# Performance work log

Hardware: AMD Instinct MI355X
Metric: run time of the kernel (lower is better)

Reference implementation:

```python
import jax, jax.numpy as jnp
import numpy as np

DN = ('NCHW', 'OIHW', 'NCHW')

def conv(x, w, b=None):
    y = jax.lax.conv_general_dilated(x, w, (1, 1), 'SAME', dimension_numbers=DN)
    if b is not None:
        y = y + b[None, :, None, None]
    return y

def bn(x, g, b, m, v, eps=1e-5):
    inv = jax.lax.rsqrt(v + eps)
    return (x - m[None, :, None, None]) * (g * inv)[None, :, None, None] + b[None, :, None, None]

def _wind_kernels():
    iso = np.array([[0.1, 0.2, 0.1], [0.2, 1.0, 0.2], [0.1, 0.2, 0.1]], np.float32)
    diag = np.array([[0.1, 0.1, 0.1], [0.1, 1.0, 0.3], [0.1, 0.1, 0.1]], np.float32)
    # directions: N, NE, E, SE, S, SW, W, NW
    ks = [iso if d in (0, 2, 4, 6) else diag for d in range(8)]
    return jnp.asarray(np.stack(ks)[:, None])  # [8,1,3,3]

def setup_inputs() -> dict:
    key = jax.random.key(0)
    ks = jax.random.split(key, 32)
    B, C, H, W = 16, 22, 256, 256
    hid = 64
    env = jax.random.normal(ks[0], (B, C, H, W), jnp.float32)
    # make wind channels realistic so the gated wind path activates
    env = env.at[:, 7].set(jax.random.uniform(ks[1], (B, H, W)) * 360.0)   # direction deg
    env = env.at[:, 8].set(jax.random.uniform(ks[2], (B, H, W)) * 20.0)    # speed
    fire0 = jax.random.uniform(ks[3], (B, 1, H, W), jnp.float32)

    def w(k, shape):
        return jax.random.normal(k, shape, jnp.float32) * 0.05

    def bnp(k, c):
        k1, k2, k3, k4 = jax.random.split(k, 4)
        return (1.0 + 0.1 * jax.random.normal(k1, (c,)),
                0.1 * jax.random.normal(k2, (c,)),
                0.1 * jax.random.normal(k3, (c,)),
                0.5 + jax.random.uniform(k4, (c,)))

    g1, be1, m1, v1 = bnp(ks[6], hid)
    g2, be2, m2, v2 = bnp(ks[7], hid)
    cg1, cbe1, cm1, cv1 = bnp(ks[8], hid)
    cg2, cbe2, cm2, cv2 = bnp(ks[9], hid // 2)
    return dict(
        env_features=env, initial_fire_state=fire0,
        w1=w(ks[10], (hid, C, 3, 3)), b1=w(ks[11], (hid,)),
        g1=g1, be1=be1, m1=m1, v1=v1,
        w2=w(ks[12], (hid, hid, 3, 3)), b2=w(ks[13], (hid,)),
        g2=g2, be2=be2, m2=m2, v2=v2,
        cw1=w(ks[14], (hid, hid + 4, 3, 3)), cb1=w(ks[15], (hid,)),
        cg1=cg1, cbe1=cbe1, cm1=cm1, cv1=cv1,
        cw2=w(ks[16], (hid // 2, hid, 3, 3)), cb2=w(ks[17], (hid // 2,)),
        cg2=cg2, cbe2=cbe2, cm2=cm2, cv2=cv2,
        cw3=w(ks[18], (4, hid // 2, 1, 1)), cb3=w(ks[19], (4,)),
        wind_k=_wind_kernels(),
        num_steps=5,
    )

def reference(env_features, initial_fire_state,
              w1, b1, g1, be1, m1, v1,
              w2, b2, g2, be2, m2, v2,
              cw1, cb1, cg1, cbe1, cm1, cv1,
              cw2, cb2, cg2, cbe2, cm2, cv2,
              cw3, cb3, wind_k, num_steps):
    # env encoder
    env = jax.nn.relu(bn(conv(env_features, w1, b1), g1, be1, m1, v1))
    env = jax.nn.relu(bn(conv(env, w2, b2), g2, be2, m2, v2))

    # per-batch wind gating: fully vectorized over batch x 8 directions
    wind_angle = env_features[:, 7].mean(axis=(1, 2))            # [B]
    wind_speed = env_features[:, 8].mean(axis=(1, 2))            # [B]
    dir_angles = jnp.arange(8, dtype=jnp.float32) * 45.0         # [8]
    diff = jnp.abs(wind_angle[:, None] - dir_angles[None, :])
    diff = jnp.minimum(diff, 360.0 - diff)
    dw = jnp.maximum(0.0, 1.0 - diff / 90.0)                     # [B,8]
    ws = jnp.clip(wind_speed / 20.0, 0.0, 1.0)                   # [B]
    gate = (dw > 0.1) & (ws[:, None] > 0.1)
    eff = jnp.where(gate, dw * ws[:, None], 0.0)                 # [B,8]

    fire_state = initial_fire_state
    evolution = [fire_state]
    for _ in range(num_steps):
        # encode fire state as one-hot of {unburned, burning, burned, water}
        idx = jnp.where(fire_state < 0.25, 0, jnp.where(fire_state < 0.75, 1, 2))
        one_hot = jax.nn.one_hot(idx[:, 0], 4, dtype=fire_state.dtype)  # [B,H,W,4]
        one_hot = jnp.transpose(one_hot, (0, 3, 1, 2))                  # [B,4,H,W]

        ca_in = jnp.concatenate([env, one_hot], axis=1)
        h = jax.nn.relu(bn(conv(ca_in, cw1, cb1), cg1, cbe1, cm1, cv1))
        h = jax.nn.relu(bn(conv(h, cw2, cb2), cg2, cbe2, cm2, cv2))
        logits = conv(h, cw3, cb3)                                      # [B,4,H,W]
        probs = jax.nn.softmax(logits, axis=1)

        # wind influence: one batched depthwise-style conv over 8 directions
        we = conv(fire_state, wind_k)                                   # [B,8,H,W]
        wind_inf = jnp.einsum('bd,bdhw->bhw', eff, we)[:, None]         # [B,1,H,W]

        boost = jax.nn.sigmoid(wind_inf) * 0.3
        target = (probs[:, 1:2] + boost) * 0.5 + probs[:, 2:3] * 1.0
        fire_state = jnp.clip(0.7 * fire_state + 0.3 * target, 0.0, 1.0)
        evolution.append(fire_state)

    return fire_state, jnp.stack(evolution, axis=0)
```

## Files before the change

kernel.cpp:

```cpp
#include <hip/hip_runtime.h>
#include <cstdint>
#include <cstddef>


#define HWSZ 65536

typedef _Float16 f16;
typedef f16 f16x8 __attribute__((ext_vector_type(8)));
typedef f16 f16x4 __attribute__((ext_vector_type(4)));
typedef float f32x4 __attribute__((ext_vector_type(4)));

#define GLDS16(gp, lp)                                                        \
  __builtin_amdgcn_global_load_lds(                                           \
      (const __attribute__((address_space(1))) void*)(gp),                    \
      (__attribute__((address_space(3))) void*)(lp), 16, 0, 0)

__global__ void k_wprepC0(const float* __restrict__ src, f16* __restrict__ dst) {
  int i = blockIdx.x * 256 + threadIdx.x;
  if (i >= 64 * 288) return;
  int co = i / 288, k = i - co * 288;
  int tap = k >> 5, ci = k & 31;
  float v = 0.f;
  if (ci < 22) {
    v = src[(co * 22 + ci) * 9 + tap];
    if (ci == 7) v *= 64.f;
  }
  dst[i] = (f16)v;
}

__global__ void k_wprep64(const float* __restrict__ src, f16* __restrict__ dst,
                          int COUT) {
  int i = blockIdx.x * 256 + threadIdx.x;
  if (i >= COUT * 576) return;
  int co = i / 576, k = i - co * 576;
  int tap = k >> 6, ci = k & 63;
  dst[i] = (f16)src[(co * 64 + ci) * 9 + tap];
}

__global__ void k_wprepC1env(const float* __restrict__ src, f16* __restrict__ dst) {
  int i = blockIdx.x * 256 + threadIdx.x;
  if (i >= 64 * 576) return;
  int co = i / 576, k = i - co * 576;
  int tap = k >> 6, ci = k & 63;
  dst[i] = (f16)src[(co * 68 + ci) * 9 + tap];
}

__global__ void k_wprepOh(const float* __restrict__ src, f16* __restrict__ dst) {
  int i = blockIdx.x * 256 + threadIdx.x;
  if (i >= 9 * 5 * 72) return;
  int tap = i / (5 * 72), r = i - tap * (5 * 72);
  int cls = r / 72, co = r - cls * 72;
  float v = 0.f;
  if (co < 64 && cls < 4) v = src[(co * 68 + 64 + cls) * 9 + tap];
  dst[i] = (f16)v;
}

__global__ void k_wprepC1(const float* __restrict__ src, f16* __restrict__ dst) {
  int i = blockIdx.x * 256 + threadIdx.x;
  if (i >= 64 * 640) return;
  int co = i / 640, k = i - co * 640;
  float v;
  if (k < 576) {
    int tap = k >> 6, ci = k & 63;
    v = src[(co * 68 + ci) * 9 + tap];
  } else {
    int kl = k - 576;
    int oc = kl & 3, tp = kl >> 2;
    v = (tp < 9) ? src[(co * 68 + 64 + oc) * 9 + tp] : 0.f;
  }
  dst[i] = (f16)v;
}

__global__ void k_bnfuse(const float* __restrict__ g, const float* __restrict__ be,
                         const float* __restrict__ m, const float* __restrict__ v,
                         const float* __restrict__ bc, float* __restrict__ s,
                         float* __restrict__ t, int C) {
  int c = threadIdx.x;
  if (c < C) {
    float sc = g[c] * rsqrtf(v[c] + 1e-5f);
    s[c] = sc;
    t[c] = (bc[c] - m[c]) * sc + be[c];
  }
}

__global__ void k_ident(float* __restrict__ s, float* __restrict__ t) {
  int c = threadIdx.x;
  if (c < 64) { s[c] = 1.f; t[c] = 0.f; }
}

__global__ __launch_bounds__(256) void k_windpart(const float* __restrict__ env,
                                                  double* __restrict__ part) {
  int blk = blockIdx.x;
  int b = blk >> 5, j = blk & 31;
  const float4* a7 = (const float4*)(env + (((size_t)(b * 22 + 7)) << 16) + j * 2048);
  const float4* a8 = (const float4*)(env + (((size_t)(b * 22 + 8)) << 16) + j * 2048);
  int tid = threadIdx.x;
  double s7 = 0.0, s8 = 0.0;
  for (int i = tid; i < 512; i += 256) {
    float4 v = a7[i];
    s7 += (double)v.x + (double)v.y + (double)v.z + (double)v.w;
    float4 u = a8[i];
    s8 += (double)u.x + (double)u.y + (double)u.z + (double)u.w;
  }
  __shared__ double r7[256], r8[256];
  r7[tid] = s7; r8[tid] = s8;
  __syncthreads();
  for (int off = 128; off > 0; off >>= 1) {
    if (tid < off) { r7[tid] += r7[tid + off]; r8[tid] += r8[tid + off]; }
    __syncthreads();
  }
  if (tid == 0) {
    part[(b * 32 + j) * 2 + 0] = r7[0];
    part[(b * 32 + j) * 2 + 1] = r8[0];
  }
}

__global__ void k_windfin(const double* __restrict__ part,
                          const float* __restrict__ wind_k, float* __restrict__ wke) {
  int b = blockIdx.x;
  if (threadIdx.x != 0) return;
  double s7 = 0.0, s8 = 0.0;
  for (int j = 0; j < 32; ++j) {
    s7 += part[(b * 32 + j) * 2 + 0];
    s8 += part[(b * 32 + j) * 2 + 1];
  }
  float wa = (float)(s7 * (1.0 / 65536.0));
  float wsp = (float)(s8 * (1.0 / 65536.0));
  float wsc = fminf(fmaxf(wsp * (1.f / 20.f), 0.f), 1.f);
  float wk[9];
#pragma unroll
  for (int tp = 0; tp < 9; ++tp) wk[tp] = 0.f;
  for (int d = 0; d < 8; ++d) {
    float diff = fabsf(wa - 45.f * (float)d);
    diff = fminf(diff, 360.f - diff);
    float dw = fmaxf(0.f, 1.f - diff * (1.f / 90.f));
    float eff = (dw > 0.1f && wsc > 0.1f) ? dw * wsc : 0.f;
    for (int tp = 0; tp < 9; ++tp) wk[tp] += eff * wind_k[d * 9 + tp];
  }
  for (int tp = 0; tp < 9; ++tp) wke[b * 9 + tp] = wk[tp];
}

__global__ void k_copy(const float* __restrict__ src, float* __restrict__ dst) {
  int i = blockIdx.x * 256 + threadIdx.x;
  ((float4*)dst)[i] = ((const float4*)src)[i];
}

__global__ void k_border(f16* __restrict__ buf, int nimg, int C) {
  int i = blockIdx.x * 256 + threadIdx.x;
  int per = 1028 * C;
  if (i >= nimg * per) return;
  int img = i / per, r = i - img * per;
  int px = r / C, c = r - px * C;
  int h, w;
  if (px < 258) { h = 0; w = px; }
  else if (px < 516) { h = 257; w = px - 258; }
  else if (px < 772) { h = px - 515; w = 0; }
  else { h = px - 771; w = 257; }
  buf[((size_t)(img * 258 + h) * 258 + w) * C + c] = (f16)0.f;
}

__global__ __launch_bounds__(256) void k_env2h(const float* __restrict__ env,
                                               f16* __restrict__ dst, int nimg) {
  int i = blockIdx.x * 256 + threadIdx.x;
  if (i >= (nimg << 16)) return;
  int b = i >> 16, hw = i & 65535;
  int h = hw >> 8, w = hw & 255;
  const float* sp = env + (((size_t)b * 22) << 16) + hw;
  f16 o[32];
#pragma unroll
  for (int c = 0; c < 22; ++c) {
    float v = sp[(size_t)c << 16];
    if (c == 7) v *= (1.f / 64.f);
    o[c] = (f16)v;
  }
#pragma unroll
  for (int c = 22; c < 32; ++c) o[c] = (f16)0.f;
  f16* dp = dst + ((size_t)(b * 258 + h + 1) * 258 + (w + 1)) * 32;
  *(f16x8*)(dp + 0) = *(f16x8*)&o[0];
  *(f16x8*)(dp + 8) = *(f16x8*)&o[8];
  *(f16x8*)(dp + 16) = *(f16x8*)&o[16];
  *(f16x8*)(dp + 24) = *(f16x8*)&o[24];
}

__global__ void k_firemap(const float* __restrict__ fire, unsigned char* __restrict__ map,
                          int nimg) {
  int i = blockIdx.x * 256 + threadIdx.x;
  if (i >= nimg * 66564) return;
  int b = i / 66564, r = i - b * 66564;
  int h = r / 258, w = r - h * 258;
  unsigned char v = 4;
  if (h >= 1 && h <= 256 && w >= 1 && w <= 256) {
    float f = fire[((size_t)b << 16) + ((h - 1) << 8) + (w - 1)];
    v = f < 0.25f ? 0 : (f < 0.75f ? 1 : 2);
  }
  map[i] = v;
}

template <int CIN, int NCS, int NS, bool ONEHOT, bool OUTPAD, bool PXSPLIT, bool RELU>
__global__ __launch_bounds__(128, 2) void k_convM(
    const f16* __restrict__ x, const f16* __restrict__ Wp,
    const float* __restrict__ scale, const float* __restrict__ shift,
    const unsigned char* __restrict__ fmap, f16* __restrict__ y, int NB) {
  constexpr int COUT = PXSPLIT ? NCS * 16 : NCS * 32;
  constexpr int KT = NS * 32;
  constexpr int CC = CIN / 8;
  constexpr int PERROW = 34 * CC;
  constexpr int ROWE = 34 * CIN;
  constexpr int PXW = PXSPLIT ? 1 : 2;
  constexpr int NH = CIN / 32;
  constexpr int VN0 = (CIN == 64) ? 6 : 4;
  constexpr int VN1 = (CIN == 64) ? 4 : 2;

  __shared__ __align__(16) f16 xs[8][ROWE];
  __shared__ float sst[2][COUT];

  int tid = threadIdx.x;
  int lane = tid & 63;
  int l15 = lane & 15;
  int g = (lane >> 4) & 3;
  int wco = tid >> 6;

  int d = blockIdx.x;
  int hsn = NB * 8;
  int ws = d / hsn;
  int t = d - ws * hsn;
  int b = t >> 3;
  int hs = t & 7;
  int w0 = ws * 32, h0 = hs * 32;

  int co_base = PXSPLIT ? 0 : wco * NCS * 16;
  int pxg = PXSPLIT ? wco * 16 : 0;

  f16x8 Af[NCS][NS];
  {
    const f16* wb = Wp + (size_t)(co_base + l15) * KT + g * 8;
#pragma unroll
    for (int cs = 0; cs < NCS; ++cs)
#pragma unroll
      for (int s = 0; s < NS; ++s)
        Af[cs][s] = *(const f16x8*)(wb + cs * 16 * KT + s * 32);
  }
  if (tid < COUT) {
    sst[0][tid] = scale[tid];
    sst[1][tid] = shift[tid];
  }

  auto stage_row = [&](int row) {
    int rs = row > 256 ? 256 : row;
    const f16* src = x + ((size_t)(b * 258 + rs + 1) * 258 + w0) * CIN;
    f16* dst = xs[(row + 1) & 7];
    for (int c = tid; c < PERROW; c += 128) {
      int px = c / CC, cc = c - px * CC;
      int sz = (CIN == 64) ? (px & 7) : ((px >> 1) & 3);
      GLDS16(src + px * CIN + ((cc ^ sz) << 3), dst + c * 8);
    }
  };

#define PHASE_SYNC()                                                      \
  do {                                                                    \
    if (wco == 0)                                                         \
      asm volatile("s_waitcnt vmcnt(%0)" ::"i"(VN0) : "memory");          \
    else                                                                  \
      asm volatile("s_waitcnt vmcnt(%0)" ::"i"(VN1) : "memory");          \
    __builtin_amdgcn_s_barrier();                                         \
    __builtin_amdgcn_sched_barrier(0);                                    \
  } while (0)

  stage_row(h0 - 1); stage_row(h0);
  stage_row(h0 + 1); stage_row(h0 + 2);
  stage_row(h0 + 3); stage_row(h0 + 4);
  PHASE_SYNC();

#pragma unroll 1
  for (int hp = h0; hp < h0 + 32; hp += 2) {
#pragma unroll
    for (int r2 = 0; r2 < 2; ++r2) {
      stage_row(hp + 5 + r2);
      int h = hp + r2;

      f32x4 acc[NCS][PXW];
#pragma unroll
      for (int cs = 0; cs < NCS; ++cs)
#pragma unroll
        for (int p = 0; p < PXW; ++p) acc[cs][p] = (f32x4){0.f, 0.f, 0.f, 0.f};

      int ia[PXW], ib[PXW], ic[PXW];
      if (ONEHOT) {
        int ta = 2 * g, tb = ta + 1;
        int dya = ta / 3, dxa = ta - 3 * dya;
        int dyb = tb / 3, dxb = tb - 3 * dyb;
#pragma unroll
        for (int pxb = 0; pxb < PXW; ++pxb) {
          int pxa = pxg + pxb * 16 + l15;
          ia[pxb] = fmap[(size_t)(b * 258 + h + dya) * 258 + w0 + pxa + dxa];
          ib[pxb] = fmap[(size_t)(b * 258 + h + dyb) * 258 + w0 + pxa + dxb];
          ic[pxb] = fmap[(size_t)(b * 258 + h + 2) * 258 + w0 + pxa + 2];
        }
      }

      const f16* sp0 = xs[h & 7];
      const f16* sp1 = xs[(h + 1) & 7];
      const f16* sp2 = xs[(h + 2) & 7];
#pragma unroll
      for (int tap = 0; tap < 9; ++tap) {
        const int dy = tap / 3, dx = tap - 3 * (tap / 3);
        const f16* sp = (dy == 0) ? sp0 : ((dy == 1) ? sp1 : sp2);
#pragma unroll
        for (int pxb = 0; pxb < PXW; ++pxb) {
          int pxd = pxg + pxb * 16 + l15 + dx;
          int sz = (CIN == 64) ? (pxd & 7) : ((pxd >> 1) & 3);
#pragma unroll
          for (int half = 0; half < NH; ++half) {
            f16x8 bb = *(const f16x8*)(sp + pxd * CIN + (((g + 4 * half) ^ sz) << 3));
#pragma unroll
            for (int cs = 0; cs < NCS; ++cs)
              acc[cs][pxb] = __builtin_amdgcn_mfma_f32_16x16x32_f16(
                  Af[cs][tap * NH + half], bb, acc[cs][pxb], 0, 0, 0);
          }
        }
      }
      if (ONEHOT) {
#pragma unroll
        for (int pxb = 0; pxb < PXW; ++pxb) {
          f16x8 b18, b19;
#pragma unroll
          for (int j = 0; j < 4; ++j) {
            b18[j] = (f16)((ia[pxb] == j) ? 1.f : 0.f);
            b18[j + 4] = (f16)((ib[pxb] == j) ? 1.f : 0.f);
            b19[j] = (f16)((g == 0 && ic[pxb] == j) ? 1.f : 0.f);
            b19[j + 4] = (f16)0.f;
          }
#pragma unroll
          for (int cs = 0; cs < NCS; ++cs) {
            acc[cs][pxb] = __builtin_amdgcn_mfma_f32_16x16x32_f16(
                Af[cs][NS - 2], b18, acc[cs][pxb], 0, 0, 0);
            acc[cs][pxb] = __builtin_amdgcn_mfma_f32_16x16x32_f16(
                Af[cs][NS - 1], b19, acc[cs][pxb], 0, 0, 0);
          }
        }
      }
#pragma unroll
      for (int cs = 0; cs < NCS; ++cs) {
        int cb = co_base + cs * 16 + 4 * g;
        f32x4 sv = *(const f32x4*)&sst[0][cb];
        f32x4 tv = *(const f32x4*)&sst[1][cb];
#pragma unroll
        for (int pxb = 0; pxb < PXW; ++pxb) {
          int px = pxg + pxb * 16 + l15;
          f16x4 o;
#pragma unroll
          for (int r = 0; r < 4; ++r) {
            float v = acc[cs][pxb][r] * sv[r] + tv[r];
            o[r] = (f16)(RELU ? fmaxf(v, 0.f) : v);
          }
          size_t oi =
              OUTPAD ? ((size_t)(b * 258 + h + 1) * 258 + (w0 + px + 1)) * 64 + cb
                     : ((size_t)(b * 256 + h) * 256 + (w0 + px)) * COUT + cb;
          *(f16x4*)&y[oi] = o;
        }
      }
    }
    PHASE_SYNC();
  }
#undef PHASE_SYNC
}

__global__ __launch_bounds__(128, 2) void k_convF(
    const f16* __restrict__ base, const f16* __restrict__ Wp,
    const f16* __restrict__ Woh,
    const float* __restrict__ s1v, const float* __restrict__ t1v,
    const float* __restrict__ s2v, const float* __restrict__ t2v,
    const unsigned char* __restrict__ fmap, f16* __restrict__ y, int NB) {
  constexpr int NS = 18, KT = NS * 32;
  __shared__ __align__(16) f16 xs[6][34 * 64];
  __shared__ f16 tbl[9 * 5 * 72];
  __shared__ float sA[2][64];
  __shared__ float sB[2][32];

  int tid = threadIdx.x;
  int lane = tid & 63;
  int l15 = lane & 15;
  int g = (lane >> 4) & 3;
  int wco = tid >> 6;

  int d = blockIdx.x;
  int hsn = NB * 8;
  int ws = d / hsn;
  int t = d - ws * hsn;
  int b = t >> 3;
  int hs = t & 7;
  int w0 = ws * 32, h0 = hs * 32;
  int co_base = wco * 16;

  f16x8 Af[NS];
  {
    const f16* wb = Wp + (size_t)(co_base + l15) * KT + g * 8;
#pragma unroll
    for (int s = 0; s < NS; ++s) Af[s] = *(const f16x8*)(wb + s * 32);
  }
  for (int i = tid; i < 9 * 5 * 72; i += 128) tbl[i] = Woh[i];
  if (tid < 64) sA[0][tid] = s1v[tid];
  else sA[1][tid - 64] = t1v[tid - 64];
  if (tid < 32) sB[0][tid] = s2v[tid];
  else if (tid < 64) sB[1][tid - 32] = t2v[tid - 32];
  __syncthreads();

  const unsigned char* fmb = fmap + (size_t)b * 66564;

  auto stage_pair = [&](int rbase) {
    for (int c = tid; c < 544; c += 128) {
      int r2 = c >= 272 ? 1 : 0;
      int cc = c - r2 * 272;
      int px = cc >> 3, q = cc & 7;
      int row = rbase + r2;
      int col = w0 - 1 + px;
      f16* dst = &xs[(row + 1) % 6][px * 64 + ((q ^ (px & 7)) << 3)];
      if ((unsigned)row < 256u && (unsigned)col < 256u) {
        f16x8 a = *(const f16x8*)&base[(((size_t)(b * 256 + row)) * 256 + col) * 64 + q * 8];
        int cls[9];
#pragma unroll
        for (int tap = 0; tap < 9; ++tap)
          cls[tap] = fmb[(size_t)(row + tap / 3) * 258 + col + tap % 3];
#pragma unroll
        for (int tap = 0; tap < 9; ++tap)
          a = a + *(const f16x8*)&tbl[(tap * 5 + cls[tap]) * 72 + q * 8];
        f16x8 o;
#pragma unroll
        for (int j = 0; j < 8; ++j) {
          float v = (float)a[j] * sA[0][q * 8 + j] + sA[1][q * 8 + j];
          o[j] = (f16)fmaxf(v, 0.f);
        }
        *(f16x8*)dst = o;
      } else {
        f16x8 z = {};
        *(f16x8*)dst = z;
      }
    }
  };

  stage_pair(h0 - 1);
  stage_pair(h0 + 1);
  __syncthreads();

#pragma unroll 1
  for (int hp = h0; hp < h0 + 32; hp += 2) {
    int c0 = 4 * tid;
    int rM2 = c0 >= 272 ? 1 : 0;
    int ccM = c0 - rM2 * 272;
    int pxM = ccM >> 3, qM = ccM & 7;
    int rowM = hp + 3 + rM2;
    int colM = w0 - 1 + pxM;
    bool okM = ((unsigned)rowM < 256u) && ((unsigned)colM < 256u);
    f16x8 sm0 = {}, sm1 = {}, sm2 = {}, sm3 = {};
    if (okM) {
      const f16* bp = &base[(((size_t)(b * 256 + rowM)) * 256 + colM) * 64 + qM * 8];
      sm0 = *(const f16x8*)(bp + 0);
      sm1 = *(const f16x8*)(bp + 8);
      sm2 = *(const f16x8*)(bp + 16);
      sm3 = *(const f16x8*)(bp + 24);
    }
    int px4 = 0, q4 = 0, col4 = 0;
    bool ok4 = false;
    f16x8 se = {};
    if (tid < 32) {
      int cc4 = 240 + tid;
      px4 = cc4 >> 3; q4 = cc4 & 7;
      col4 = w0 - 1 + px4;
      ok4 = ((unsigned)(hp + 4) < 256u) && ((unsigned)col4 < 256u);
      if (ok4)
        se = *(const f16x8*)&base[(((size_t)(b * 256 + hp + 4)) * 256 + col4) * 64 + q4 * 8];
    }
    __builtin_amdgcn_sched_barrier(0);

#pragma unroll
    for (int rr = 0; rr < 2; ++rr) {
      int h = hp + rr;
      f32x4 acc[2];
      acc[0] = (f32x4){0.f, 0.f, 0.f, 0.f};
      acc[1] = (f32x4){0.f, 0.f, 0.f, 0.f};
      const f16* sp0 = xs[h % 6];
      const f16* sp1 = xs[(h + 1) % 6];
      const f16* sp2 = xs[(h + 2) % 6];
#pragma unroll
      for (int tap = 0; tap < 9; ++tap) {
        const int dy = tap / 3, dx = tap - 3 * (tap / 3);
        const f16* sp = (dy == 0) ? sp0 : ((dy == 1) ? sp1 : sp2);
#pragma unroll
        for (int pxb = 0; pxb < 2; ++pxb) {
          int pxd = pxb * 16 + l15 + dx;
          int sz = pxd & 7;
#pragma unroll
          for (int half = 0; half < 2; ++half) {
            f16x8 bb = *(const f16x8*)(sp + pxd * 64 + (((g + 4 * half) ^ sz) << 3));
            acc[pxb] = __builtin_amdgcn_mfma_f32_16x16x32_f16(
                Af[tap * 2 + half], bb, acc[pxb], 0, 0, 0);
          }
        }
      }
      int cb = co_base + 4 * g;
      f32x4 sv = *(const f32x4*)&sB[0][cb];
      f32x4 tv = *(const f32x4*)&sB[1][cb];
#pragma unroll
      for (int pxb = 0; pxb < 2; ++pxb) {
        int px = pxb * 16 + l15;
        f16x4 o;
#pragma unroll
        for (int r = 0; r < 4; ++r)
          o[r] = (f16)fmaxf(acc[pxb][r] * sv[r] + tv[r], 0.f);
        *(f16x4*)&y[((size_t)(b * 256 + h) * 256 + (w0 + px)) * 32 + cb] = o;
      }
    }
    __builtin_amdgcn_sched_barrier(0);

    {
      f16* dstM = &xs[(rowM + 1) % 6][pxM * 64];
      if (okM) {
        int cls[9];
#pragma unroll
        for (int tap = 0; tap < 9; ++tap)
          cls[tap] = fmb[(size_t)(rowM + tap / 3) * 258 + colM + tap % 3];
#define XFORM(SRC, QOFF)                                                      \
  {                                                                           \
    int q_ = qM + QOFF;                                                       \
    f16x8 a_ = SRC;                                                           \
    _Pragma("unroll") for (int tap = 0; tap < 9; ++tap)                       \
        a_ = a_ + *(const f16x8*)&tbl[(tap * 5 + cls[tap]) * 72 + q_ * 8];    \
    f16x8 o_;                                                                 \
    _Pragma("unroll") for (int j = 0; j < 8; ++j) {                           \
      float v_ = (float)a_[j] * sA[0][q_ * 8 + j] + sA[1][q_ * 8 + j];        \
      o_[j] = (f16)fmaxf(v_, 0.f);                                           \
    }                                                                         \
    *(f16x8*)(dstM + ((q_ ^ (pxM & 7)) << 3)) = o_;                           \
  }
        XFORM(sm0, 0)
        XFORM(sm1, 1)
        XFORM(sm2, 2)
        XFORM(sm3, 3)
#undef XFORM
      } else {
        f16x8 z = {};
        *(f16x8*)(dstM + (((qM + 0) ^ (pxM & 7)) << 3)) = z;
        *(f16x8*)(dstM + (((qM + 1) ^ (pxM & 7)) << 3)) = z;
        *(f16x8*)(dstM + (((qM + 2) ^ (pxM & 7)) << 3)) = z;
        *(f16x8*)(dstM + (((qM + 3) ^ (pxM & 7)) << 3)) = z;
      }
      if (tid < 32) {
        f16* dst4 = &xs[(hp + 5) % 6][px4 * 64 + ((q4 ^ (px4 & 7)) << 3)];
        if (ok4) {
          int cls[9];
#pragma unroll
          for (int tap = 0; tap < 9; ++tap)
            cls[tap] = fmb[(size_t)(hp + 4 + tap / 3) * 258 + col4 + tap % 3];
          f16x8 a_ = se;
#pragma unroll
          for (int tap = 0; tap < 9; ++tap)
            a_ = a_ + *(const f16x8*)&tbl[(tap * 5 + cls[tap]) * 72 + q4 * 8];
          f16x8 o_;
#pragma unroll
          for (int j = 0; j < 8; ++j) {
            float v_ = (float)a_[j] * sA[0][q4 * 8 + j] + sA[1][q4 * 8 + j];
            o_[j] = (f16)fmaxf(v_, 0.f);
          }
          *(f16x8*)dst4 = o_;
        } else {
          f16x8 z = {};
          *(f16x8*)dst4 = z;
        }
      }
    }
    __syncthreads();
  }
}

__global__ __launch_bounds__(256) void k_step(
    const f16* __restrict__ h2, const float* __restrict__ cw3,
    const float* __restrict__ cb3, const float* __restrict__ wke,
    const float* __restrict__ fin, float* __restrict__ fout,
    float* __restrict__ fout2, unsigned char* __restrict__ mapout) {
  __shared__ float wl[4][32];
  __shared__ float bl[4];
  __shared__ float wk[9];
  int tid = threadIdx.x;
  if (tid < 128) wl[tid >> 5][tid & 31] = cw3[tid];
  if (tid < 4) bl[tid] = cb3[tid];
  int bx = blockIdx.x;
  int b = bx >> 8, h = bx & 255;
  if (tid < 9) wk[tid] = wke[b * 9 + tid];
  __syncthreads();
  int w = tid;
  const f16x8* hp8 = (const f16x8*)(h2 + ((size_t)(b * 256 + h) * 256 + w) * 32);
  float l0 = bl[0], l1 = bl[1], l2 = bl[2], l3 = bl[3];
#pragma unroll
  for (int q = 0; q < 4; ++q) {
    f16x8 v8 = hp8[q];
#pragma unroll
    for (int j = 0; j < 8; ++j) {
      float v = (float)v8[j];
      int c = q * 8 + j;
      l0 += v * wl[0][c];
      l1 += v * wl[1][c];
      l2 += v * wl[2][c];
      l3 += v * wl[3][c];
    }
  }
  float mx = fmaxf(fmaxf(l0, l1), fmaxf(l2, l3));
  float e0 = expf(l0 - mx), e1 = expf(l1 - mx), e2 = expf(l2 - mx), e3 = expf(l3 - mx);
  float inv = 1.f / (e0 + e1 + e2 + e3);
  float p1 = e1 * inv, p2 = e2 * inv;
  const float* fp = fin + ((size_t)b << 16);
  float wacc = 0.f;
#pragma unroll
  for (int tap = 0; tap < 9; ++tap) {
    int dy = tap / 3 - 1, dx = tap % 3 - 1;
    int hh = h + dy, ww2 = w + dx;
    float f = ((unsigned)hh < 256u && (unsigned)ww2 < 256u) ? fp[(hh << 8) + ww2] : 0.f;
    wacc += wk[tap] * f;
  }
  float boost = 0.3f / (1.f + expf(-wacc));
  float fcur = fp[(h << 8) + w];
  float target = 0.5f * p1 + 0.5f * boost + p2;
  float fn = 0.7f * fcur + 0.3f * target;
  fn = fminf(fmaxf(fn, 0.f), 1.f);
  size_t o = ((size_t)b << 16) + (h << 8) + w;
  fout[o] = fn;
  if (fout2) fout2[o] = fn;
  mapout[(size_t)(b * 258 + h + 1) * 258 + (w + 1)] =
      fn < 0.25f ? (unsigned char)0 : (fn < 0.75f ? (unsigned char)1 : (unsigned char)2);
}

extern "C" void kernel_launch(void* const* d_in, const int* in_sizes, int n_in,
                              void* d_out, int out_size, void* d_ws, size_t ws_size,
                              hipStream_t stream) {
  const float* env = (const float*)d_in[0];
  const float* fire0 = (const float*)d_in[1];
  const float* w1 = (const float*)d_in[2];
  const float* b1 = (const float*)d_in[3];
  const float* g1 = (const float*)d_in[4];
  const float* be1 = (const float*)d_in[5];
  const float* m1 = (const float*)d_in[6];
  const float* v1 = (const float*)d_in[7];
  const float* w2 = (const float*)d_in[8];
  const float* b2 = (const float*)d_in[9];
  const float* g2 = (const float*)d_in[10];
  const float* be2 = (const float*)d_in[11];
  const float* m2 = (const float*)d_in[12];
  const float* v2 = (const float*)d_in[13];
  const float* cw1 = (const float*)d_in[14];
  const float* cb1 = (const float*)d_in[15];
  const float* cg1 = (const float*)d_in[16];
  const float* cbe1 = (const float*)d_in[17];
  const float* cm1 = (const float*)d_in[18];
  const float* cv1 = (const float*)d_in[19];
  const float* cw2 = (const float*)d_in[20];
  const float* cb2 = (const float*)d_in[21];
  const float* cg2 = (const float*)d_in[22];
  const float* cbe2 = (const float*)d_in[23];
  const float* cm2 = (const float*)d_in[24];
  const float* cv2 = (const float*)d_in[25];
  const float* cw3 = (const float*)d_in[26];
  const float* cb3 = (const float*)d_in[27];
  const float* windk = (const float*)d_in[28];

  float* out = (float*)d_out;
  float* evo = out + 1048576;

  uint8_t* p = (uint8_t*)d_ws;
  f16* W1p = (f16*)p;           p += 64 * 288 * 2;
  f16* W2p = (f16*)p;           p += 64 * 576 * 2;
  f16* Wc1p = (f16*)p;          p += 64 * 640 * 2;
  f16* Wenv = (f16*)p;          p += 64 * 576 * 2;
  f16* Woh = (f16*)p;           p += 9 * 5 * 72 * 2;
  f16* Wc2p = (f16*)p;          p += 32 * 576 * 2;
  float* s1 = (float*)p;        p += 64 * 4;
  float* t1 = (float*)p;        p += 64 * 4;
  float* s2 = (float*)p;        p += 64 * 4;
  float* t2 = (float*)p;        p += 64 * 4;
  float* sc1 = (float*)p;       p += 64 * 4;
  float* tc1 = (float*)p;       p += 64 * 4;
  float* sc2 = (float*)p;       p += 64 * 4;
  float* tc2 = (float*)p;       p += 64 * 4;
  float* idsc = (float*)p;      p += 64 * 4;
  float* idsh = (float*)p;      p += 64 * 4;
  float* wke = (float*)p;       p += 1024;
  double* wpart = (double*)p;   p += 16 * 32 * 2 * 8;
  unsigned char* fmap = p;      p += 16 * 66564 + 1024;

  const size_t IMGP = (size_t)258 * 258 * 64;
  const size_t IMGP32 = (size_t)258 * 258 * 32;
  const size_t IMGU = (size_t)65536 * 64;
  const size_t S = 16 * IMGP * 2;
  const size_t CH64 = IMGP * 2;
  const size_t CH32 = IMGP32 * 2;
  size_t fixed = (size_t)(p - (uint8_t*)d_ws);

  bool basePath = false;
  int NB = 1;
  for (int nb = 16; nb >= 1; nb >>= 1) {
    if (fixed + 2 * S + (size_t)nb * CH32 <= ws_size) { basePath = true; NB = nb; break; }
  }
  if (!basePath) {
    for (int nb = 16; nb >= 1; nb >>= 1) {
      size_t need = fixed + S + (size_t)nb * (CH64 + CH32);
      if (need <= ws_size) { NB = nb; break; }
    }
  }

  k_wprepC0<<<(64 * 288 + 255) / 256, 256, 0, stream>>>(w1, W1p);
  k_wprep64<<<(64 * 576 + 255) / 256, 256, 0, stream>>>(w2, W2p, 64);
  k_wprep64<<<(32 * 576 + 255) / 256, 256, 0, stream>>>(cw2, Wc2p, 32);
  k_bnfuse<<<1, 256, 0, stream>>>(g1, be1, m1, v1, b1, s1, t1, 64);
  k_bnfuse<<<1, 256, 0, stream>>>(g2, be2, m2, v2, b2, s2, t2, 64);
  k_bnfuse<<<1, 256, 0, stream>>>(cg1, cbe1, cm1, cv1, cb1, sc1, tc1, 64);
  k_bnfuse<<<1, 256, 0, stream>>>(cg2, cbe2, cm2, cv2, cb2, sc2, tc2, 32);
  k_windpart<<<512, 256, 0, stream>>>(env, wpart);
  k_windfin<<<16, 64, 0, stream>>>(wpart, windk, wke);
  k_copy<<<1024, 256, 0, stream>>>(fire0, evo);
  k_firemap<<<(16 * 66564 + 255) / 256, 256, 0, stream>>>(fire0, fmap, 16);

  if (basePath) {
    k_wprepC1env<<<(64 * 576 + 255) / 256, 256, 0, stream>>>(cw1, Wenv);
    k_wprepOh<<<(9 * 5 * 72 + 255) / 256, 256, 0, stream>>>(cw1, Woh);
    k_ident<<<1, 64, 0, stream>>>(idsc, idsh);

    f16* S1 = (f16*)(p);
    f16* S2 = (f16*)(p + S);
    f16* chunk = (f16*)(p + 2 * S);
    f16* envin = chunk;
    f16* h2 = chunk;

    k_border<<<(16 * 1028 * 64 + 255) / 256, 256, 0, stream>>>(S1, 16, 64);
    k_border<<<(16 * 1028 * 64 + 255) / 256, 256, 0, stream>>>(S2, 16, 64);
    k_border<<<(NB * 1028 * 32 + 255) / 256, 256, 0, stream>>>(envin, NB, 32);

    const int gconv = NB * 64;
    for (int b0 = 0; b0 < 16; b0 += NB) {
      k_env2h<<<NB * 256, 256, 0, stream>>>(env + (size_t)b0 * 22 * HWSZ, envin, NB);
      k_convM<32, 2, 9, false, true, false, true><<<gconv, 128, 0, stream>>>(
          envin, W1p, s1, t1, nullptr, S1 + (size_t)b0 * IMGP, NB);
      k_convM<64, 2, 18, false, true, false, true><<<gconv, 128, 0, stream>>>(
          S1 + (size_t)b0 * IMGP, W2p, s2, t2, nullptr, S2 + (size_t)b0 * IMGP, NB);
      k_convM<64, 2, 18, false, false, false, false><<<gconv, 128, 0, stream>>>(
          S2 + (size_t)b0 * IMGP, Wenv, idsc, idsh, nullptr,
          S1 + (size_t)b0 * IMGU, NB);
    }
    for (int t = 0; t < 5; ++t) {
      const float* fin = evo + (size_t)t * 1048576;
      float* fo = evo + (size_t)(t + 1) * 1048576;
      for (int b0 = 0; b0 < 16; b0 += NB) {
        k_convF<<<gconv, 128, 0, stream>>>(
            S1 + (size_t)b0 * IMGU, Wc2p, Woh, sc1, tc1, sc2, tc2,
            fmap + (size_t)b0 * 66564, h2, NB);
        k_step<<<NB * 256, 256, 0, stream>>>(
            h2, cw3, cb3, wke + (size_t)b0 * 9, fin + (size_t)b0 * HWSZ,
            fo + (size_t)b0 * HWSZ, (t == 4) ? out + (size_t)b0 * HWSZ : nullptr,
            fmap + (size_t)b0 * 66564);
      }
    }
  } else {
    k_wprepC1<<<(64 * 640 + 255) / 256, 256, 0, stream>>>(cw1, Wc1p);
    f16* envf = (f16*)p;
    f16* h1p = (f16*)(p + S);
    f16* chunk = (f16*)(p + S + (size_t)NB * CH64);
    f16* envin = chunk;
    f16* h2 = chunk;

    k_border<<<(16 * 1028 * 64 + 255) / 256, 256, 0, stream>>>(envf, 16, 64);
    k_border<<<(NB * 1028 * 64 + 255) / 256, 256, 0, stream>>>(h1p, NB, 64);
    k_border<<<(NB * 1028 * 32 + 255) / 256, 256, 0, stream>>>(envin, NB, 32);

    const int gconv = NB * 64;
    for (int b0 = 0; b0 < 16; b0 += NB) {
      k_env2h<<<NB * 256, 256, 0, stream>>>(env + (size_t)b0 * 22 * HWSZ, envin, NB);
      k_convM<32, 2, 9, false, true, false, true><<<gconv, 128, 0, stream>>>(
          envin, W1p, s1, t1, nullptr, h1p, NB);
      k_convM<64, 2, 18, false, true, false, true><<<gconv, 128, 0, stream>>>(
          h1p, W2p, s2, t2, nullptr, envf + (size_t)b0 * IMGP, NB);
    }
    for (int t = 0; t < 5; ++t) {
      const float* fin = evo + (size_t)t * 1048576;
      float* fo = evo + (size_t)(t + 1) * 1048576;
      for (int b0 = 0; b0 < 16; b0 += NB) {
        k_convM<64, 2, 20, true, true, false, true><<<gconv, 128, 0, stream>>>(
            envf + (size_t)b0 * IMGP, Wc1p, sc1, tc1, fmap + (size_t)b0 * 66564,
            h1p, NB);
        k_convM<64, 2, 18, false, false, true, true><<<gconv, 128, 0, stream>>>(
            h1p, Wc2p, sc2, tc2, nullptr, h2, NB);
        k_step<<<NB * 256, 256, 0, stream>>>(
            h2, cw3, cb3, wke + (size_t)b0 * 9, fin + (size_t)b0 * HWSZ,
            fo + (size_t)b0 * HWSZ, (t == 4) ? out + (size_t)b0 * HWSZ : nullptr,
            fmap + (size_t)b0 * 66564);
      }
    }
  }
}
```

Baseline: 855.0 us.

## Split conv work across four waves per block with one output tile per wave

Adds a 256-thread k_convM4 variant in which each of four waves computes 16 output channels over the full 32-pixel row tile. It stages eight rows ahead through async global-to-LDS loads with per-wave vmcnt waits. k_convF also moves to 256 threads, splitting work as 2 channel groups times 2 pixel halves so each wave holds one accumulator, and its halo staging is simplified into shared load and transform helpers. The goal is more waves per CU to hide latency and less register pressure per wave. The cost is more threads contending for LDS and barriers, plus weight fragments reloaded per wave.

Result: slower. 1.779 ms (+108.0%).

```diff
diff --git a/kernel.cpp b/kernel.cpp
--- a/kernel.cpp
+++ b/kernel.cpp
@@ -194,6 +194,128 @@
     v = f < 0.25f ? 0 : (f < 0.75f ? 1 : 2);
   }
   map[i] = v;
+}
+
+template <int CIN, int NS, bool OUTPAD, bool RELU>
+__global__ __launch_bounds__(256, 4) void k_convM4(
+    const f16* __restrict__ x, const f16* __restrict__ Wp,
+    const float* __restrict__ scale, const float* __restrict__ shift,
+    f16* __restrict__ y, int NB) {
+  constexpr int KT = NS * 32;
+  constexpr int CC = CIN / 8;
+  constexpr int PERROW = 34 * CC;
+  constexpr int ROWE = 34 * CIN;
+  constexpr int NH = CIN / 32;
+  constexpr int NST = 4;
+  constexpr int SGA = (CIN == 64) ? 4 : 2;
+  constexpr int SGB = (CIN == 64) ? 2 : 0;
+
+  __shared__ __align__(16) f16 xs[8][ROWE];
+  __shared__ float sst[2][64];
+
+  int tid = threadIdx.x;
+  int lane = tid & 63;
+  int l15 = lane & 15;
+  int g = (lane >> 4) & 3;
+  int wid = tid >> 6;
+  bool lead = (CIN == 64) ? (wid == 0) : (wid < 3);
+  int co_base = wid * 16;
+
+  int d = blockIdx.x;
+  int hsn = NB * 8;
+  int ws = d / hsn;
+  int t = d - ws * hsn;
+  int b = t >> 3;
+  int hs = t & 7;
+  int w0 = ws * 32, h0 = hs * 32;
+
+  f16x8 Af[NS];
+  {
+    const f16* wb = Wp + (size_t)(co_base + l15) * KT + g * 8;
+#pragma unroll
+    for (int s = 0; s < NS; ++s) Af[s] = *(const f16x8*)(wb + s * 32);
+  }
+  if (tid < 64) sst[0][tid] = scale[tid];
+  else if (tid < 128) sst[1][tid - 64] = shift[tid - 64];
+
+  auto stage_row = [&](int row) {
+    int rs = row > 256 ? 256 : row;
+    const f16* src = x + ((size_t)(b * 258 + rs + 1) * 258 + w0) * CIN;
+    f16* dst = xs[(row + 1) & 7];
+    for (int c = tid; c < PERROW; c += 256) {
+      int px = c / CC, cc = c - px * CC;
+      int sz = (CIN == 64) ? (px & 7) : ((px >> 1) & 3);
+      GLDS16(src + px * CIN + ((cc ^ sz) << 3), dst + c * 8);
+    }
+  };
+
+#define PHASE_SYNC(NA, NBW)                                               \
+  do {                                                                    \
+    if (lead)                                                             \
+      asm volatile("s_waitcnt vmcnt(%0)" ::"i"(NA) : "memory");           \
+    else                                                                  \
+      asm volatile("s_waitcnt vmcnt(%0)" ::"i"(NBW) : "memory");          \
+    __builtin_amdgcn_s_barrier();                                         \
+    __builtin_amdgcn_sched_barrier(0);                                    \
+  } while (0)
+
+  stage_row(h0 - 1); stage_row(h0);
+  stage_row(h0 + 1); stage_row(h0 + 2);
+  stage_row(h0 + 3); stage_row(h0 + 4);
+  PHASE_SYNC(SGA, SGB);
+
+#pragma unroll 1
+  for (int hp = h0; hp < h0 + 32; hp += 2) {
+    stage_row(hp + 5);
+    stage_row(hp + 6);
+    __builtin_amdgcn_sched_barrier(0);
+
+#pragma unroll
+    for (int rr = 0; rr < 2; ++rr) {
+      int h = hp + rr;
+      f32x4 acc[2];
+      acc[0] = (f32x4){0.f, 0.f, 0.f, 0.f};
+      acc[1] = (f32x4){0.f, 0.f, 0.f, 0.f};
+      const f16* sp0 = xs[h & 7];
+      const f16* sp1 = xs[(h + 1) & 7];
+      const f16* sp2 = xs[(h + 2) & 7];
+#pragma unroll
+      for (int tap = 0; tap < 9; ++tap) {
+        const int dy = tap / 3, dx = tap - 3 * (tap / 3);
+        const f16* sp = (dy == 0) ? sp0 : ((dy == 1) ? sp1 : sp2);
+#pragma unroll
+        for (int pxb = 0; pxb < 2; ++pxb) {
+          int pxd = pxb * 16 + l15 + dx;
+          int sz = (CIN == 64) ? (pxd & 7) : ((pxd >> 1) & 3);
+#pragma unroll
+          for (int half = 0; half < NH; ++half) {
+            f16x8 bb = *(const f16x8*)(sp + pxd * CIN + (((g + 4 * half) ^ sz) << 3));
+            acc[pxb] = __builtin_amdgcn_mfma_f32_16x16x32_f16(
+                Af[tap * NH + half], bb, acc[pxb], 0, 0, 0);
+          }
+        }
+      }
+      int cb = co_base + 4 * g;
+      f32x4 sv = *(const f32x4*)&sst[0][cb];
+      f32x4 tv = *(const f32x4*)&sst[1][cb];
+#pragma unroll
+      for (int pxb = 0; pxb < 2; ++pxb) {
+        int px = pxb * 16 + l15;
+        f16x4 o;
+#pragma unroll
+        for (int r = 0; r < 4; ++r) {
+          float v = acc[pxb][r] * sv[r] + tv[r];
+          o[r] = (f16)(RELU ? fmaxf(v, 0.f) : v);
+        }
+        size_t oi =
+            OUTPAD ? ((size_t)(b * 258 + h + 1) * 258 + (w0 + px + 1)) * 64 + cb
+                   : ((size_t)(b * 256 + h) * 256 + (w0 + px)) * 64 + cb;
+        *(f16x4*)&y[oi] = o;
+      }
+    }
+    PHASE_SYNC(SGA + NST, SGB + NST);
+  }
+#undef PHASE_SYNC
 }
 
 template <int CIN, int NCS, int NS, bool ONEHOT, bool OUTPAD, bool PXSPLIT, bool RELU>
@@ -365,7 +487,7 @@
 #undef PHASE_SYNC
 }
 
-__global__ __launch_bounds__(128, 2) void k_convF(
+__global__ __launch_bounds__(256, 4) void k_convF(
     const f16* __restrict__ base, const f16* __restrict__ Wp,
     const f16* __restrict__ Woh,
     const float* __restrict__ s1v, const float* __restrict__ t1v,
@@ -381,7 +503,9 @@
   int lane = tid & 63;
   int l15 = lane & 15;
   int g = (lane >> 4) & 3;
-  int wco = tid >> 6;
+  int wid = tid >> 6;
+  int co_base = (wid & 1) * 16;
+  int pxg = (wid >> 1) * 16;
 
   int d = blockIdx.x;
   int hsn = NB * 8;
@@ -390,7 +514,6 @@
   int b = t >> 3;
   int hs = t & 7;
   int w0 = ws * 32, h0 = hs * 32;
-  int co_base = wco * 16;
 
   f16x8 Af[NS];
   {
@@ -398,86 +521,68 @@
 #pragma unroll
     for (int s = 0; s < NS; ++s) Af[s] = *(const f16x8*)(wb + s * 32);
   }
-  for (int i = tid; i < 9 * 5 * 72; i += 128) tbl[i] = Woh[i];
+  for (int i = tid; i < 9 * 5 * 72; i += 256) tbl[i] = Woh[i];
   if (tid < 64) sA[0][tid] = s1v[tid];
-  else sA[1][tid - 64] = t1v[tid - 64];
-  if (tid < 32) sB[0][tid] = s2v[tid];
-  else if (tid < 64) sB[1][tid - 32] = t2v[tid - 32];
+  else if (tid < 128) sA[1][tid - 64] = t1v[tid - 64];
+  else if (tid < 160) sB[0][tid - 128] = s2v[tid - 128];
+  else if (tid < 192) sB[1][tid - 160] = t2v[tid - 160];
   __syncthreads();
 
   const unsigned char* fmb = fmap + (size_t)b * 66564;
 
-  auto stage_pair = [&](int rbase) {
-    for (int c = tid; c < 544; c += 128) {
-      int r2 = c >= 272 ? 1 : 0;
-      int cc = c - r2 * 272;
-      int px = cc >> 3, q = cc & 7;
-      int row = rbase + r2;
-      int col = w0 - 1 + px;
-      f16* dst = &xs[(row + 1) % 6][px * 64 + ((q ^ (px & 7)) << 3)];
-      if ((unsigned)row < 256u && (unsigned)col < 256u) {
-        f16x8 a = *(const f16x8*)&base[(((size_t)(b * 256 + row)) * 256 + col) * 64 + q * 8];
-        int cls[9];
-#pragma unroll
-        for (int tap = 0; tap < 9; ++tap)
-          cls[tap] = fmb[(size_t)(row + tap / 3) * 258 + col + tap % 3];
-#pragma unroll
-        for (int tap = 0; tap < 9; ++tap)
-          a = a + *(const f16x8*)&tbl[(tap * 5 + cls[tap]) * 72 + q * 8];
-        f16x8 o;
-#pragma unroll
-        for (int j = 0; j < 8; ++j) {
-          float v = (float)a[j] * sA[0][q * 8 + j] + sA[1][q * 8 + j];
-          o[j] = (f16)fmaxf(v, 0.f);
-        }
-        *(f16x8*)dst = o;
-      } else {
-        f16x8 z = {};
-        *(f16x8*)dst = z;
-      }
-    }
+  auto ldchunk = [&](int c, int rb) -> f16x8 {
+    int r2 = c >= 272 ? 1 : 0;
+    int cc = c - r2 * 272;
+    int px = cc >> 3, q = cc & 7;
+    int row = rb + r2, col = w0 - 1 + px;
+    if ((unsigned)row < 256u && (unsigned)col < 256u)
+      return *(const f16x8*)&base[(((size_t)(b * 256 + row)) * 256 + col) * 64 + q * 8];
+    f16x8 z = {};
+    return z;
   };
-
-  stage_pair(h0 - 1);
-  stage_pair(h0 + 1);
+  auto xform = [&](int c, int rb, f16x8 a) {
+    int r2 = c >= 272 ? 1 : 0;
+    int cc = c - r2 * 272;
+    int px = cc >> 3, q = cc & 7;
+    int row = rb + r2, col = w0 - 1 + px;
+    f16* dst = &xs[(row + 1) % 6][px * 64 + ((q ^ (px & 7)) << 3)];
+    if ((unsigned)row < 256u && (unsigned)col < 256u) {
+      int cls[9];
+#pragma unroll
+      for (int tap = 0; tap < 9; ++tap)
+        cls[tap] = fmb[(size_t)(row + tap / 3) * 258 + col + tap % 3];
+#pragma unroll
+      for (int tap = 0; tap < 9; ++tap)
+        a = a + *(const f16x8*)&tbl[(tap * 5 + cls[tap]) * 72 + q * 8];
+      f16x8 o;
+#pragma unroll
+      for (int j = 0; j < 8; ++j) {
+        float v = (float)a[j] * sA[0][q * 8 + j] + sA[1][q * 8 + j];
+        o[j] = (f16)fmaxf(v, 0.f);
+      }
+      *(f16x8*)dst = o;
+    } else {
+      f16x8 z = {};
+      *(f16x8*)dst = z;
+    }
+  };
+
+  for (int rb = h0 - 1; rb <= h0 + 1; rb += 2)
+    for (int c = tid; c < 544; c += 256) xform(c, rb, ldchunk(c, rb));
   __syncthreads();
 
 #pragma unroll 1
   for (int hp = h0; hp < h0 + 32; hp += 2) {
-    int c0 = 4 * tid;
-    int rM2 = c0 >= 272 ? 1 : 0;
-    int ccM = c0 - rM2 * 272;
-    int pxM = ccM >> 3, qM = ccM & 7;
-    int rowM = hp + 3 + rM2;
-    int colM = w0 - 1 + pxM;
-    bool okM = ((unsigned)rowM < 256u) && ((unsigned)colM < 256u);
-    f16x8 sm0 = {}, sm1 = {}, sm2 = {}, sm3 = {};
-    if (okM) {
-      const f16* bp = &base[(((size_t)(b * 256 + rowM)) * 256 + colM) * 64 + qM * 8];
-      sm0 = *(const f16x8*)(bp + 0);
-      sm1 = *(const f16x8*)(bp + 8);
-      sm2 = *(const f16x8*)(bp + 16);
-      sm3 = *(const f16x8*)(bp + 24);
-    }
-    int px4 = 0, q4 = 0, col4 = 0;
-    bool ok4 = false;
-    f16x8 se = {};
-    if (tid < 32) {
-      int cc4 = 240 + tid;
-      px4 = cc4 >> 3; q4 = cc4 & 7;
-      col4 = w0 - 1 + px4;
-      ok4 = ((unsigned)(hp + 4) < 256u) && ((unsigned)col4 < 256u);
-      if (ok4)
-        se = *(const f16x8*)&base[(((size_t)(b * 256 + hp + 4)) * 256 + col4) * 64 + q4 * 8];
-    }
+    f16x8 la = ldchunk(tid, hp + 3);
+    f16x8 lb = ldchunk(tid + 256, hp + 3);
+    f16x8 lc = {};
+    if (tid < 32) lc = ldchunk(tid + 512, hp + 3);
     __builtin_amdgcn_sched_barrier(0);
 
 #pragma unroll
     for (int rr = 0; rr < 2; ++rr) {
       int h = hp + rr;
-      f32x4 acc[2];
-      acc[0] = (f32x4){0.f, 0.f, 0.f, 0.f};
-      acc[1] = (f32x4){0.f, 0.f, 0.f, 0.f};
+      f32x4 acc = (f32x4){0.f, 0.f, 0.f, 0.f};
       const f16* sp0 = xs[h % 6];
       const f16* sp1 = xs[(h + 1) % 6];
       const f16* sp2 = xs[(h + 2) % 6];
@@ -485,89 +590,29 @@
       for (int tap = 0; tap < 9; ++tap) {
         const int dy = tap / 3, dx = tap - 3 * (tap / 3);
         const f16* sp = (dy == 0) ? sp0 : ((dy == 1) ? sp1 : sp2);
-#pragma unroll
-        for (int pxb = 0; pxb < 2; ++pxb) {
-          int pxd = pxb * 16 + l15 + dx;
-          int sz = pxd & 7;
-#pragma unroll
-          for (int half = 0; half < 2; ++half) {
-            f16x8 bb = *(const f16x8*)(sp + pxd * 64 + (((g + 4 * half) ^ sz) << 3));
-            acc[pxb] = __builtin_amdgcn_mfma_f32_16x16x32_f16(
-                Af[tap * 2 + half], bb, acc[pxb], 0, 0, 0);
-          }
+        int pxd = pxg + l15 + dx;
+        int sz = pxd & 7;
+#pragma unroll
+        for (int half = 0; half < 2; ++half) {
+          f16x8 bb = *(const f16x8*)(sp + pxd * 64 + (((g + 4 * half) ^ sz) << 3));
+          acc = __builtin_amdgcn_mfma_f32_16x16x32_f16(Af[tap * 2 + half], bb, acc,
+                                                       0, 0, 0);
         }
       }
       int cb = co_base + 4 * g;
       f32x4 sv = *(const f32x4*)&sB[0][cb];
       f32x4 tv = *(const f32x4*)&sB[1][cb];
-#pragma unroll
-      for (int pxb = 0; pxb < 2; ++pxb) {
-        int px = pxb * 16 + l15;
-        f16x4 o;
-#pragma unroll
-        for (int r = 0; r < 4; ++r)
-          o[r] = (f16)fmaxf(acc[pxb][r] * sv[r] + tv[r], 0.f);
-        *(f16x4*)&y[((size_t)(b * 256 + h) * 256 + (w0 + px)) * 32 + cb] = o;
-      }
+      f16x4 o;
+#pragma unroll
+      for (int r = 0; r < 4; ++r)
+        o[r] = (f16)fmaxf(acc[r] * sv[r] + tv[r], 0.f);
+      *(f16x4*)&y[((size_t)(b * 256 + h) * 256 + (w0 + pxg + l15)) * 32 + cb] = o;
     }
     __builtin_amdgcn_sched_barrier(0);
 
-    {
-      f16* dstM = &xs[(rowM + 1) % 6][pxM * 64];
-      if (okM) {
-        int cls[9];
-#pragma unroll
-        for (int tap = 0; tap < 9; ++tap)
-          cls[tap] = fmb[(size_t)(rowM + tap / 3) * 258 + colM + tap % 3];
-#define XFORM(SRC, QOFF)                                                      \
-  {                                                                           \
-    int q_ = qM + QOFF;                                                       \
-    f16x8 a_ = SRC;                                                           \
-    _Pragma("unroll") for (int tap = 0; tap < 9; ++tap)                       \
-        a_ = a_ + *(const f16x8*)&tbl[(tap * 5 + cls[tap]) * 72 + q_ * 8];    \
-    f16x8 o_;                                                                 \
-    _Pragma("unroll") for (int j = 0; j < 8; ++j) {                           \
-      float v_ = (float)a_[j] * sA[0][q_ * 8 + j] + sA[1][q_ * 8 + j];        \
-      o_[j] = (f16)fmaxf(v_, 0.f);                                           \
-    }                                                                         \
-    *(f16x8*)(dstM + ((q_ ^ (pxM & 7)) << 3)) = o_;                           \
-  }
-        XFORM(sm0, 0)
-        XFORM(sm1, 1)
-        XFORM(sm2, 2)
-        XFORM(sm3, 3)
-#undef XFORM
-      } else {
-        f16x8 z = {};
-        *(f16x8*)(dstM + (((qM + 0) ^ (pxM & 7)) << 3)) = z;
-        *(f16x8*)(dstM + (((qM + 1) ^ (pxM & 7)) << 3)) = z;
-        *(f16x8*)(dstM + (((qM + 2) ^ (pxM & 7)) << 3)) = z;
-        *(f16x8*)(dstM + (((qM + 3) ^ (pxM & 7)) << 3)) = z;
-      }
-      if (tid < 32) {
-        f16* dst4 = &xs[(hp + 5) % 6][px4 * 64 + ((q4 ^ (px4 & 7)) << 3)];
-        if (ok4) {
-          int cls[9];
-#pragma unroll
-          for (int tap = 0; tap < 9; ++tap)
-            cls[tap] = fmb[(size_t)(hp + 4 + tap / 3) * 258 + col4 + tap % 3];
-          f16x8 a_ = se;
-#pragma unroll
-          for (int tap = 0; tap < 9; ++tap)
-            a_ = a_ + *(const f16x8*)&tbl[(tap * 5 + cls[tap]) * 72 + q4 * 8];
-          f16x8 o_;
-#pragma unroll
-          for (int j = 0; j < 8; ++j) {
-            float v_ = (float)a_[j] * sA[0][q4 * 8 + j] + sA[1][q4 * 8 + j];
-            o_[j] = (f16)fmaxf(v_, 0.f);
-          }
-          *(f16x8*)dst4 = o_;
-        } else {
-          f16x8 z = {};
-          *(f16x8*)dst4 = z;
-        }
-      }
-    }
+    xform(tid, hp + 3, la);
+    xform(tid + 256, hp + 3, lb);
+    if (tid < 32) xform(tid + 512, hp + 3, lc);
     __syncthreads();
   }
 }
@@ -735,19 +780,18 @@
     const int gconv = NB * 64;
     for (int b0 = 0; b0 < 16; b0 += NB) {
       k_env2h<<<NB * 256, 256, 0, stream>>>(env + (size_t)b0 * 22 * HWSZ, envin, NB);
-      k_convM<32, 2, 9, false, true, false, true><<<gconv, 128, 0, stream>>>(
-          envin, W1p, s1, t1, nullptr, S1 + (size_t)b0 * IMGP, NB);
-      k_convM<64, 2, 18, false, true, false, true><<<gconv, 128, 0, stream>>>(
-          S1 + (size_t)b0 * IMGP, W2p, s2, t2, nullptr, S2 + (size_t)b0 * IMGP, NB);
-      k_convM<64, 2, 18, false, false, false, false><<<gconv, 128, 0, stream>>>(
-          S2 + (size_t)b0 * IMGP, Wenv, idsc, idsh, nullptr,
-          S1 + (size_t)b0 * IMGU, NB);
+      k_convM4<32, 9, true, true><<<gconv, 256, 0, stream>>>(
+          envin, W1p, s1, t1, S1 + (size_t)b0 * IMGP, NB);
+      k_convM4<64, 18, true, true><<<gconv, 256, 0, stream>>>(
+          S1 + (size_t)b0 * IMGP, W2p, s2, t2, S2 + (size_t)b0 * IMGP, NB);
+      k_convM4<64, 18, false, false><<<gconv, 256, 0, stream>>>(
+          S2 + (size_t)b0 * IMGP, Wenv, idsc, idsh, S1 + (size_t)b0 * IMGU, NB);
     }
     for (int t = 0; t < 5; ++t) {
       const float* fin = evo + (size_t)t * 1048576;
       float* fo = evo + (size_t)(t + 1) * 1048576;
       for (int b0 = 0; b0 < 16; b0 += NB) {
-        k_convF<<<gconv, 128, 0, stream>>>(
+        k_convF<<<gconv, 256, 0, stream>>>(
             S1 + (size_t)b0 * IMGU, Wc2p, Woh, sc1, tc1, sc2, tc2,
             fmap + (size_t)b0 * 66564, h2, NB);
         k_step<<<NB * 256, 256, 0, stream>>>(
```
